# Kernel tuning notes

Measured on AMD Instinct MI355X. Metric: run time of the kernel, lower is better.

The kernel has to match this reference:

```python
import jax, jax.numpy as jnp
import numpy as np

TAU = 2.0          # LIF membrane time constant (spikingjelly default)
ALPHA = 2.0        # ATan surrogate width
EPS = 1e-5         # BatchNorm eps
NUM_HEADS = 8
SCALE = 0.125

@jax.custom_vjp
def spike(x):
    return (x >= 0.0).astype(x.dtype)

def _spike_fwd(x):
    return (x >= 0.0).astype(x.dtype), x

def _spike_bwd(x, g):
    # ATan surrogate gradient (spikingjelly default)
    return (g * (ALPHA / 2.0) / (1.0 + (jnp.pi / 2.0 * ALPHA * x) ** 2),)

spike.defvjp(_spike_fwd, _spike_bwd)

def lif(x, v_th):
    # Multi-step LIF over leading time axis T; hard reset to 0, v_reset=0.
    def step(v, xt):
        h = v + (xt - v) / TAU
        s = spike(h - v_th)
        return h * (1.0 - s), s
    _, s = jax.lax.scan(step, jnp.zeros_like(x[0]), x)
    return s

def bn(x, g, b, m, v):
    # BatchNorm1d in eval mode over channel (last) dim
    return (x - m) * jax.lax.rsqrt(v + EPS) * g + b

def setup_inputs() -> dict:
    key = jax.random.key(0)
    ks = jax.random.split(key, 16)
    T, B, N, C = 4, 16, 512, 512
    s = 1.0 / np.sqrt(C)
    inp = {"x": jax.random.normal(ks[0], (T, B, N, C), jnp.float32)}
    for i, p in enumerate("qkvp"):
        inp[f"w{p}"] = jax.random.normal(ks[1 + i], (C, C), jnp.float32) * s
        inp[f"b{p}"] = jnp.zeros((C,), jnp.float32)
        inp[f"{p}_gamma"] = jnp.ones((C,), jnp.float32)
        inp[f"{p}_beta"] = jnp.zeros((C,), jnp.float32)
        inp[f"{p}_mean"] = jax.random.normal(ks[5 + i], (C,), jnp.float32) * 0.1
        inp[f"{p}_var"] = jax.random.uniform(ks[9 + i], (C,), jnp.float32, minval=0.5, maxval=1.5)
    return inp

def reference(x, wq, bq, q_gamma, q_beta, q_mean, q_var,
              wk, bk, k_gamma, k_beta, k_mean, k_var,
              wv, bv, v_gamma, v_beta, v_mean, v_var,
              wp, bp, p_gamma, p_beta, p_mean, p_var):
    T, B, N, C = x.shape
    H = NUM_HEADS
    D = C // H

    def branch(w, b, g, be, m, va):
        y = bn(x @ w.T + b, g, be, m, va)          # Linear -> BN1d (eval)
        y = lif(y, 1.0)                             # spiking activation
        return y.reshape(T, B, N, H, D).transpose(0, 1, 3, 2, 4)  # [T,B,H,N,D]

    q = branch(wq, bq, q_gamma, q_beta, q_mean, q_var)
    k = branch(wk, bk, k_gamma, k_beta, k_mean, k_var)
    v = branch(wv, bv, v_gamma, v_beta, v_mean, v_var)

    attn = jnp.einsum('tbhnd,tbhmd->tbhnm', q, k) * SCALE  # [T,B,H,N,N]
    o = jnp.einsum('tbhnm,tbhmd->tbhnd', attn, v)          # [T,B,H,N,D]
    o = o.transpose(0, 1, 3, 2, 4).reshape(T, B, N, C)
    o = lif(o, 0.5)                                        # attn_lif, v_th=0.5
    o = bn(o @ wp.T + bp, p_gamma, p_beta, p_mean, p_var)
    return lif(o, 1.0)
```

## Files before the change

kernel.cpp:

```cpp
#include <hip/hip_runtime.h>
#include <hip/hip_bf16.h>
#include <hip/hip_fp16.h>
#include <cstddef>
#include <cstdint>

#define T_ 4
#define B_ 16
#define N_ 512
#define C_ 512
#define H_ 8
#define D_ 64
#define BN_T (B_*N_)

typedef unsigned short u16;
typedef __attribute__((ext_vector_type(8))) short bf16x8;
typedef __attribute__((ext_vector_type(8))) _Float16 f16x8;
typedef __attribute__((ext_vector_type(8))) unsigned short u16x8;
typedef __attribute__((ext_vector_type(4))) float f32x4;

__device__ __forceinline__ u16 f2bf_exact(float f) {
    union { float f; unsigned u; } x; x.f = f; return (u16)(x.u >> 16);
}
__device__ __forceinline__ void split2(float f, u16& h1, u16& h2) {
    const __half a = __float2half(f);
    const float r = (f - __half2float(a)) * 2048.0f;
    const __half b = __float2half(r);
    h1 = __half_as_ushort(a); h2 = __half_as_ushort(b);
}
__device__ __forceinline__ int swz(int rr, int q) {
    return (rr << 6) + (((q ^ ((rr >> 1) & 3)) & 3) << 4);
}
__device__ __forceinline__ int SW(int row, int col) {
    return (row << 6) + (col ^ ((row & 7) << 3));
}
__device__ __forceinline__ void gload16(const void* g, void* l) {
    __builtin_amdgcn_global_load_lds(
        (const __attribute__((address_space(1))) unsigned int*)g,
        (__attribute__((address_space(3))) unsigned int*)l, 16, 0, 0);
}

__global__ __launch_bounds__(256) void k_split_x(
    const float* __restrict__ x, u16* __restrict__ x1t, u16* __restrict__ x2t)
{
    const int tile = blockIdx.x;
    const int mt = tile >> 4, kb = tile & 15;
    const int tid = threadIdx.x;
    const int rr = tid >> 1, kh = tid & 1;
    const int t = rr & 3, bn = mt * 32 + (rr >> 2);
    const float* src = x + ((size_t)t * BN_T + bn) * C_ + kb * 32 + kh * 16;
    float f[16];
    *reinterpret_cast<float4*>(f + 0)  = *reinterpret_cast<const float4*>(src + 0);
    *reinterpret_cast<float4*>(f + 4)  = *reinterpret_cast<const float4*>(src + 4);
    *reinterpret_cast<float4*>(f + 8)  = *reinterpret_cast<const float4*>(src + 8);
    *reinterpret_cast<float4*>(f + 12) = *reinterpret_cast<const float4*>(src + 12);
    char* d1 = (char*)(x1t + ((size_t)tile << 12));
    char* d2 = (char*)(x2t + ((size_t)tile << 12));
    #pragma unroll
    for (int j = 0; j < 2; ++j) {
        u16x8 p1, p2;
        #pragma unroll
        for (int e = 0; e < 8; ++e) { u16 h1, h2; split2(f[8*j+e], h1, h2); p1[e] = h1; p2[e] = h2; }
        const int q = 2 * kh + j;
        *reinterpret_cast<u16x8*>(d1 + swz(rr, q)) = p1;
        *reinterpret_cast<u16x8*>(d2 + swz(rr, q)) = p2;
    }
}

__global__ __launch_bounds__(256) void k_split_w(
    const float* __restrict__ w, u16* __restrict__ w1t, u16* __restrict__ w2t)
{
    const int tile = blockIdx.x;
    const int nt = tile >> 4, kb = tile & 15;
    const int tid = threadIdx.x;
    const int rr = tid >> 1, kh = tid & 1;
    const int c = nt * 128 + rr;
    const float* src = w + (size_t)c * C_ + kb * 32 + kh * 16;
    float f[16];
    *reinterpret_cast<float4*>(f + 0)  = *reinterpret_cast<const float4*>(src + 0);
    *reinterpret_cast<float4*>(f + 4)  = *reinterpret_cast<const float4*>(src + 4);
    *reinterpret_cast<float4*>(f + 8)  = *reinterpret_cast<const float4*>(src + 8);
    *reinterpret_cast<float4*>(f + 12) = *reinterpret_cast<const float4*>(src + 12);
    char* d1 = (char*)(w1t + ((size_t)tile << 12));
    char* d2 = (char*)(w2t + ((size_t)tile << 12));
    #pragma unroll
    for (int j = 0; j < 2; ++j) {
        u16x8 p1, p2;
        #pragma unroll
        for (int e = 0; e < 8; ++e) { u16 h1, h2; split2(f[8*j+e], h1, h2); p1[e] = h1; p2[e] = h2; }
        const int q = 2 * kh + j;
        *reinterpret_cast<u16x8*>(d1 + swz(rr, q)) = p1;
        *reinterpret_cast<u16x8*>(d2 + swz(rr, q)) = p2;
    }
}

__global__ __launch_bounds__(256, 2) void k_linear_qkv(
    const u16* __restrict__ a1t, const u16* __restrict__ a2t,
    const u16* __restrict__ wt_base,
    const float* __restrict__ bi0, const float* __restrict__ ga0, const float* __restrict__ be0,
    const float* __restrict__ mu0, const float* __restrict__ va0,
    const float* __restrict__ bi1, const float* __restrict__ ga1, const float* __restrict__ be1,
    const float* __restrict__ mu1, const float* __restrict__ va1,
    const float* __restrict__ bi2, const float* __restrict__ ga2, const float* __restrict__ be2,
    const float* __restrict__ mu2, const float* __restrict__ va2,
    u16* __restrict__ oq, u16* __restrict__ ok, u16* __restrict__ ov)
{
    __shared__ u16 lds[2][2][4096];

    const int dd  = blockIdx.x;
    const int lid = (dd & 7) * 384 + (dd >> 3);
    const int mt  = lid / 12;
    const int ntg = lid - mt * 12;
    const int li  = ntg >> 2;
    const int nt  = ntg & 3;
    const int bn0 = mt * 32;
    const int c0  = nt * 128;

    const float* bias  = li == 0 ? bi0 : li == 1 ? bi1 : bi2;
    const float* gamma = li == 0 ? ga0 : li == 1 ? ga1 : ga2;
    const float* beta  = li == 0 ? be0 : li == 1 ? be1 : be2;
    const float* mean  = li == 0 ? mu0 : li == 1 ? mu1 : mu2;
    const float* var   = li == 0 ? va0 : li == 1 ? va1 : va2;
    u16* outp = li == 0 ? oq : li == 1 ? ok : ov;

    const size_t WSZ = (size_t)C_ * C_;
    const u16* w1t = wt_base + (size_t)(2 * li) * WSZ;
    const u16* w2t = wt_base + (size_t)(2 * li + 1) * WSZ;

    const int tid = threadIdx.x;
    const int wv  = tid >> 6, lane = tid & 63;
    const int l15 = tid & 15, g = (tid & 63) >> 4;
    const int wr  = wv >> 1, wc = wv & 1;
    const int go  = wv * 2048 + lane * 16;
    const int lo  = wv * 2048;

    f32x4 accA[4][4], accB[4][4];
    #pragma unroll
    for (int rt = 0; rt < 4; ++rt)
        #pragma unroll
        for (int ct = 0; ct < 4; ++ct) { accA[rt][ct] = {0,0,0,0}; accB[rt][ct] = {0,0,0,0}; }

    const size_t abase = (size_t)mt * 16, bbase = (size_t)nt * 16;

    auto stage = [&](int buf, int kb) {
        char* L = (char*)&lds[buf][0][0];
        const char* gb1 = (const char*)(w1t + ((bbase + kb) << 12)) + go;
        const char* gb2 = (const char*)(w2t + ((bbase + kb) << 12)) + go;
        gload16(gb1,        L + lo);
        gload16(gb1 + 1024, L + lo + 1024);
        gload16(gb2,        L + 8192 + lo);
        gload16(gb2 + 1024, L + 8192 + lo + 1024);
    };
    auto lda = [&](int kb, f16x8 (&a1)[4], f16x8 (&a2)[4]) {
        const char* t1 = (const char*)(a1t + ((abase + kb) << 12));
        const char* t2 = (const char*)(a2t + ((abase + kb) << 12));
        #pragma unroll
        for (int rt = 0; rt < 4; ++rt) {
            const int rr = 64 * wr + 16 * rt + l15;
            a1[rt] = *reinterpret_cast<const f16x8*>(t1 + swz(rr, g));
            a2[rt] = *reinterpret_cast<const f16x8*>(t2 + swz(rr, g));
        }
    };
    auto comp = [&](int buf, const f16x8 (&a1)[4], const f16x8 (&a2)[4]) {
        const char* L = (const char*)&lds[buf][0][0];
        #pragma unroll
        for (int ct = 0; ct < 4; ++ct) {
            const int rr2 = 64 * wc + 16 * ct + l15;
            const f16x8 b1 = *reinterpret_cast<const f16x8*>(L + swz(rr2, g));
            const f16x8 b2 = *reinterpret_cast<const f16x8*>(L + 8192 + swz(rr2, g));
            #pragma unroll
            for (int rt = 0; rt < 4; ++rt) {
                accA[rt][ct] = __builtin_amdgcn_mfma_f32_16x16x32_f16(a1[rt], b1, accA[rt][ct], 0, 0, 0);
                accB[rt][ct] = __builtin_amdgcn_mfma_f32_16x16x32_f16(a2[rt], b1, accB[rt][ct], 0, 0, 0);
                accB[rt][ct] = __builtin_amdgcn_mfma_f32_16x16x32_f16(a1[rt], b2, accB[rt][ct], 0, 0, 0);
            }
        }
    };

    f16x8 aE1[4], aE2[4], aO1[4], aO2[4];
    lda(0, aE1, aE2);
    stage(0, 0);
    __syncthreads();

    #pragma unroll 1
    for (int kb = 0; kb < 16; kb += 2) {
        lda(kb + 1, aO1, aO2);
        stage(1, kb + 1);
        comp(0, aE1, aE2);
        __syncthreads();
        if (kb + 2 < 16) { lda(kb + 2, aE1, aE2); stage(0, kb + 2); }
        comp(1, aO1, aO2);
        __syncthreads();
    }

    #pragma unroll
    for (int ct = 0; ct < 4; ++ct) {
        const int c = c0 + 64 * wc + 16 * ct + l15;
        const float rs = 1.0f / sqrtf(var[c] + 1e-5f);
        const float ga = gamma[c], be = beta[c], mu = mean[c], bi = bias[c];
        #pragma unroll
        for (int rt = 0; rt < 4; ++rt) {
            const int bn = bn0 + 16 * wr + 4 * rt + g;
            float vm = 0.f;
            #pragma unroll
            for (int r = 0; r < 4; ++r) {
                const float y = accA[rt][ct][r] + accB[rt][ct][r] * (1.0f / 2048.0f) + bi;
                const float ybn = (y - mu) * rs * ga + be;
                const float h = vm + (ybn - vm) * 0.5f;
                const bool sp = (h >= 1.0f);
                vm = sp ? 0.f : h;
                const int b = bn >> 9, n = bn & 511;
                const int hh = c >> 6, d2 = c & 63;
                outp[((((size_t)r * B_ + b) * H_ + hh) * N_ + n) * D_ + d2] = sp ? 0x3F80 : 0;
            }
        }
    }
}

__global__ __launch_bounds__(256, 2) void k_linear_out(
    const u16* __restrict__ a1t,
    const u16* __restrict__ w1t, const u16* __restrict__ w2t,
    const float* __restrict__ bias, const float* __restrict__ gamma,
    const float* __restrict__ beta, const float* __restrict__ mean,
    const float* __restrict__ var, float* __restrict__ outp)
{
    __shared__ u16 lds[2][2][4096];

    const int dd  = blockIdx.x;
    const int lid = (dd & 7) * 128 + (dd >> 3);
    const int mt  = lid >> 2;
    const int nt  = lid & 3;
    const int bn0 = mt * 32;
    const int c0  = nt * 128;

    const int tid = threadIdx.x;
    const int wv  = tid >> 6, lane = tid & 63;
    const int l15 = tid & 15, g = (tid & 63) >> 4;
    const int wr  = wv >> 1, wc = wv & 1;
    const int go  = wv * 2048 + lane * 16;
    const int lo  = wv * 2048;

    f32x4 accA[4][4], accB[4][4];
    #pragma unroll
    for (int rt = 0; rt < 4; ++rt)
        #pragma unroll
        for (int ct = 0; ct < 4; ++ct) { accA[rt][ct] = {0,0,0,0}; accB[rt][ct] = {0,0,0,0}; }

    const size_t abase = (size_t)mt * 16, bbase = (size_t)nt * 16;

    auto stage = [&](int buf, int kb) {
        char* L = (char*)&lds[buf][0][0];
        const char* gb1 = (const char*)(w1t + ((bbase + kb) << 12)) + go;
        const char* gb2 = (const char*)(w2t + ((bbase + kb) << 12)) + go;
        gload16(gb1,        L + lo);
        gload16(gb1 + 1024, L + lo + 1024);
        gload16(gb2,        L + 8192 + lo);
        gload16(gb2 + 1024, L + 8192 + lo + 1024);
    };
    auto lda = [&](int kb, f16x8 (&a1)[4]) {
        const char* t1 = (const char*)(a1t + ((abase + kb) << 12));
        #pragma unroll
        for (int rt = 0; rt < 4; ++rt) {
            const int rr = 64 * wr + 16 * rt + l15;
            a1[rt] = *reinterpret_cast<const f16x8*>(t1 + swz(rr, g));
        }
    };
    auto comp = [&](int buf, const f16x8 (&a1)[4]) {
        const char* L = (const char*)&lds[buf][0][0];
        #pragma unroll
        for (int ct = 0; ct < 4; ++ct) {
            const int rr2 = 64 * wc + 16 * ct + l15;
            const f16x8 b1 = *reinterpret_cast<const f16x8*>(L + swz(rr2, g));
            const f16x8 b2 = *reinterpret_cast<const f16x8*>(L + 8192 + swz(rr2, g));
            #pragma unroll
            for (int rt = 0; rt < 4; ++rt) {
                accA[rt][ct] = __builtin_amdgcn_mfma_f32_16x16x32_f16(a1[rt], b1, accA[rt][ct], 0, 0, 0);
                accB[rt][ct] = __builtin_amdgcn_mfma_f32_16x16x32_f16(a1[rt], b2, accB[rt][ct], 0, 0, 0);
            }
        }
    };

    f16x8 aE1[4], aO1[4];
    lda(0, aE1);
    stage(0, 0);
    __syncthreads();

    #pragma unroll 1
    for (int kb = 0; kb < 16; kb += 2) {
        lda(kb + 1, aO1);
        stage(1, kb + 1);
        comp(0, aE1);
        __syncthreads();
        if (kb + 2 < 16) { lda(kb + 2, aE1); stage(0, kb + 2); }
        comp(1, aO1);
        __syncthreads();
    }

    #pragma unroll
    for (int ct = 0; ct < 4; ++ct) {
        const int c = c0 + 64 * wc + 16 * ct + l15;
        const float rs = 1.0f / sqrtf(var[c] + 1e-5f);
        const float ga = gamma[c], be = beta[c], mu = mean[c], bi = bias[c];
        #pragma unroll
        for (int rt = 0; rt < 4; ++rt) {
            const int bn = bn0 + 16 * wr + 4 * rt + g;
            float vm = 0.f;
            #pragma unroll
            for (int r = 0; r < 4; ++r) {
                const float y = accA[rt][ct][r] + accB[rt][ct][r] * (1.0f / 2048.0f) + bi;
                const float ybn = (y - mu) * rs * ga + be;
                const float h = vm + (ybn - vm) * 0.5f;
                const bool sp = (h >= 1.0f);
                vm = sp ? 0.f : h;
                outp[((size_t)r * BN_T + bn) * C_ + c] = sp ? 1.0f : 0.0f;
            }
        }
    }
}

__global__ __launch_bounds__(512, 2) void k_attn_mfma(
    const u16* __restrict__ qg, const u16* __restrict__ kg,
    const u16* __restrict__ vg, u16* __restrict__ s2t)
{
    __shared__ u16 kf[8][4096];
    __shared__ u16 vf[8][4096];
    __shared__ u16 ssb[8][1024];

    const int id  = blockIdx.x;
    const int lid = (id & 7) * 64 + (id >> 3);
    const int bh  = lid >> 2;
    const int qt  = lid & 3;
    const int b   = bh >> 3, hh = bh & 7;

    const int tid  = threadIdx.x;
    const int w    = tid >> 6, lane = tid & 63;
    const int l15  = lane & 15, g = lane >> 4;

    const int vkv = (tid & 15) * 4;
    const int vd  = ((tid >> 4) & 15) * 4;

    bf16x8 qa[2];
    f32x4 vmem[4], oacc[4];
    #pragma unroll
    for (int d0 = 0; d0 < 4; ++d0) { vmem[d0] = {0,0,0,0}; oacc[d0] = {0,0,0,0}; }

    #pragma unroll 1
    for (int t = 0; t < T_; ++t) {
        const size_t base = ((size_t)t * (B_ * H_) + bh) * (size_t)(N_ * D_);
        if (t > 0) __syncthreads();

        {
            const size_t qrow = base + (size_t)(qt * 128 + 16 * w + l15) * D_;
            qa[0] = *reinterpret_cast<const bf16x8*>(qg + qrow + 8 * g);
            qa[1] = *reinterpret_cast<const bf16x8*>(qg + qrow + 32 + 8 * g);
        }
        {
            const u16* kb = kg + base;
            #pragma unroll
            for (int i = 0; i < 8; ++i) {
                const int r64 = tid >> 3;
                const int col = (tid & 7) * 8;
                const u16x8 v = *reinterpret_cast<const u16x8*>(kb + ((size_t)(tid + 512 * i)) * 8);
                *reinterpret_cast<u16x8*>(&kf[i][SW(r64, col)]) = v;
            }
        }
        {
            const u16* vb = vg + base;
            #pragma unroll
            for (int i = 0; i < 4; ++i) {
                const int jt = 2 * i + (tid >> 8);
                const int m0 = jt * 64;
                ushort4 r0 = *reinterpret_cast<const ushort4*>(vb + (size_t)(m0 + vkv + 0) * D_ + vd);
                ushort4 r1 = *reinterpret_cast<const ushort4*>(vb + (size_t)(m0 + vkv + 1) * D_ + vd);
                ushort4 r2 = *reinterpret_cast<const ushort4*>(vb + (size_t)(m0 + vkv + 2) * D_ + vd);
                ushort4 r3 = *reinterpret_cast<const ushort4*>(vb + (size_t)(m0 + vkv + 3) * D_ + vd);
                ushort4 wv4;
                wv4.x = r0.x; wv4.y = r1.x; wv4.z = r2.x; wv4.w = r3.x;
                *reinterpret_cast<ushort4*>(&vf[jt][SW(vd + 0, vkv)]) = wv4;
                wv4.x = r0.y; wv4.y = r1.y; wv4.z = r2.y; wv4.w = r3.y;
                *reinterpret_cast<ushort4*>(&vf[jt][SW(vd + 1, vkv)]) = wv4;
                wv4.x = r0.z; wv4.y = r1.z; wv4.z = r2.z; wv4.w = r3.z;
                *reinterpret_cast<ushort4*>(&vf[jt][SW(vd + 2, vkv)]) = wv4;
                wv4.x = r0.w; wv4.y = r1.w; wv4.z = r2.w; wv4.w = r3.w;
                *reinterpret_cast<ushort4*>(&vf[jt][SW(vd + 3, vkv)]) = wv4;
            }
        }
        __syncthreads();

        u16* sb = &ssb[w][0];
        #pragma unroll
        for (int jt = 0; jt < 8; ++jt) {
            __builtin_amdgcn_s_setprio(1);
            #pragma unroll
            for (int kvt = 0; kvt < 2; ++kvt) {
                f32x4 acc = {0.f, 0.f, 0.f, 0.f};
                #pragma unroll
                for (int c = 0; c < 2; ++c) {
                    const bf16x8 kb = *reinterpret_cast<const bf16x8*>(
                        &kf[jt][SW(16 * kvt + l15, 32 * c + 8 * g)]);
                    acc = __builtin_amdgcn_mfma_f32_16x16x32_bf16(qa[c], kb, acc, 0, 0, 0);
                }
                #pragma unroll
                for (int r = 0; r < 4; ++r)
                    sb[SW(4 * g + r, 16 * kvt + l15)] = f2bf_exact(acc[r]);
            }
            {
                const bf16x8 sa = *reinterpret_cast<const bf16x8*>(&sb[SW(l15, 8 * g)]);
                #pragma unroll
                for (int d0 = 0; d0 < 4; ++d0) {
                    const bf16x8 vb2 = *reinterpret_cast<const bf16x8*>(
                        &vf[jt][SW(16 * d0 + l15, 8 * g)]);
                    oacc[d0] = __builtin_amdgcn_mfma_f32_16x16x32_bf16(sa, vb2, oacc[d0], 0, 0, 0);
                }
            }
            #pragma unroll
            for (int kvt = 2; kvt < 4; ++kvt) {
                f32x4 acc = {0.f, 0.f, 0.f, 0.f};
                #pragma unroll
                for (int c = 0; c < 2; ++c) {
                    const bf16x8 kb = *reinterpret_cast<const bf16x8*>(
                        &kf[jt][SW(16 * kvt + l15, 32 * c + 8 * g)]);
                    acc = __builtin_amdgcn_mfma_f32_16x16x32_bf16(qa[c], kb, acc, 0, 0, 0);
                }
                #pragma unroll
                for (int r = 0; r < 4; ++r)
                    sb[SW(4 * g + r, 16 * kvt + l15)] = f2bf_exact(acc[r]);
            }
            {
                const bf16x8 sa = *reinterpret_cast<const bf16x8*>(&sb[SW(l15, 32 + 8 * g)]);
                #pragma unroll
                for (int d0 = 0; d0 < 4; ++d0) {
                    const bf16x8 vb2 = *reinterpret_cast<const bf16x8*>(
                        &vf[jt][SW(16 * d0 + l15, 32 + 8 * g)]);
                    oacc[d0] = __builtin_amdgcn_mfma_f32_16x16x32_bf16(sa, vb2, oacc[d0], 0, 0, 0);
                }
            }
            __builtin_amdgcn_s_setprio(0);
        }

        #pragma unroll
        for (int d0 = 0; d0 < 4; ++d0) {
            const int c = hh * 64 + d0 * 16 + l15;
            const int kb2 = c >> 5, kq = (c >> 3) & 3, e = c & 7;
            #pragma unroll
            for (int r = 0; r < 4; ++r) {
                const float o = oacc[d0][r] * 0.125f;
                const float h = vmem[d0][r] + (o - vmem[d0][r]) * 0.5f;
                const bool sp = (h >= 0.5f);
                vmem[d0][r] = sp ? 0.f : h;
                const int n = qt * 128 + 16 * w + 4 * g + r;
                const int bn = b * 512 + n;
                const int mt2 = bn >> 5;
                const int rr2 = (bn & 31) * 4 + t;
                const size_t off = (((size_t)mt2 * 16 + kb2) << 13) + (rr2 << 6)
                                 + (((kq ^ ((rr2 >> 1) & 3)) & 3) << 4) + (e << 1);
                *(u16*)((char*)s2t + off) = sp ? 0x3C00 : 0;
            }
            oacc[d0] = {0.f, 0.f, 0.f, 0.f};
        }
    }
}

extern "C" void kernel_launch(void* const* d_in, const int* in_sizes, int n_in,
                              void* d_out, int out_size, void* d_ws, size_t ws_size,
                              hipStream_t stream)
{
    const float* x = (const float*)d_in[0];
    const float* W[4]  = {(const float*)d_in[1],  (const float*)d_in[7],  (const float*)d_in[13], (const float*)d_in[19]};
    const float* Bi[4] = {(const float*)d_in[2],  (const float*)d_in[8],  (const float*)d_in[14], (const float*)d_in[20]};
    const float* Ga[4] = {(const float*)d_in[3],  (const float*)d_in[9],  (const float*)d_in[15], (const float*)d_in[21]};
    const float* Be[4] = {(const float*)d_in[4],  (const float*)d_in[10], (const float*)d_in[16], (const float*)d_in[22]};
    const float* Mu[4] = {(const float*)d_in[5],  (const float*)d_in[11], (const float*)d_in[17], (const float*)d_in[23]};
    const float* Va[4] = {(const float*)d_in[6],  (const float*)d_in[12], (const float*)d_in[18], (const float*)d_in[24]};

    const size_t SPK = (size_t)T_ * B_ * N_ * C_;
    const size_t WSZ = (size_t)C_ * C_;
    u16* qb  = (u16*)d_ws;
    u16* kbf = qb + SPK;
    u16* vbf = kbf + SPK;
    u16* x1t = vbf + SPK;
    u16* x2t = x1t + SPK;
    u16* wt  = x2t + SPK;
    u16* s2t = x1t;

    dim3 blk(256);
    k_split_x<<<4096, blk, 0, stream>>>(x, x1t, x2t);
    for (int i = 0; i < 4; ++i)
        k_split_w<<<64, blk, 0, stream>>>(W[i], wt + (2*i) * WSZ, wt + (2*i+1) * WSZ);

    k_linear_qkv<<<3072, blk, 0, stream>>>(x1t, x2t, wt,
        Bi[0], Ga[0], Be[0], Mu[0], Va[0],
        Bi[1], Ga[1], Be[1], Mu[1], Va[1],
        Bi[2], Ga[2], Be[2], Mu[2], Va[2],
        qb, kbf, vbf);
    k_attn_mfma<<<512, dim3(512), 0, stream>>>(qb, kbf, vbf, s2t);
    k_linear_out<<<1024, blk, 0, stream>>>(s2t, wt + 6*WSZ, wt + 7*WSZ,
        Bi[3], Ga[3], Be[3], Mu[3], Va[3], (float*)d_out);
}
```

Baseline: 305.4 us.

## Widen linear GEMM tiles to 512 threads with triple-buffered LDS pipeline

Both linear kernels now use 512-thread blocks covering 256 output columns, so each block reuses its A tile across twice as many columns. The A operand is staged through LDS alongside the split weights instead of being read directly from global memory into registers. The double-buffered loop becomes a three-stage ring using explicit vmcnt waits, raw s_barrier and setprio around the MFMA loops, so global loads overlap compute more deeply. The cost is much more LDS per block (up to 144 KB for qkv), which may limit occupancy, plus the risk of fragile hand-written waitcnt counts.

```diff
diff --git a/kernel.cpp b/kernel.cpp
--- a/kernel.cpp
+++ b/kernel.cpp
@@ -93,7 +93,7 @@
     }
 }
 
-__global__ __launch_bounds__(256, 2) void k_linear_qkv(
+__global__ __launch_bounds__(512, 2) void k_linear_qkv(
     const u16* __restrict__ a1t, const u16* __restrict__ a2t,
     const u16* __restrict__ wt_base,
     const float* __restrict__ bi0, const float* __restrict__ ga0, const float* __restrict__ be0,
@@ -104,16 +104,16 @@
     const float* __restrict__ mu2, const float* __restrict__ va2,
     u16* __restrict__ oq, u16* __restrict__ ok, u16* __restrict__ ov)
 {
-    __shared__ u16 lds[2][2][4096];
+    __shared__ u16 lds[3][6][4096];
 
     const int dd  = blockIdx.x;
-    const int lid = (dd & 7) * 384 + (dd >> 3);
-    const int mt  = lid / 12;
-    const int ntg = lid - mt * 12;
-    const int li  = ntg >> 2;
-    const int nt  = ntg & 3;
+    const int lid = (dd & 7) * 192 + (dd >> 3);
+    const int mt  = lid / 6;
+    const int rem = lid - mt * 6;
+    const int li  = rem >> 1;
+    const int nt  = rem & 1;
     const int bn0 = mt * 32;
-    const int c0  = nt * 128;
+    const int c0  = nt * 256;
 
     const float* bias  = li == 0 ? bi0 : li == 1 ? bi1 : bi2;
     const float* gamma = li == 0 ? ga0 : li == 1 ? ga1 : ga2;
@@ -128,10 +128,9 @@
 
     const int tid = threadIdx.x;
     const int wv  = tid >> 6, lane = tid & 63;
-    const int l15 = tid & 15, g = (tid & 63) >> 4;
-    const int wr  = wv >> 1, wc = wv & 1;
-    const int go  = wv * 2048 + lane * 16;
-    const int lo  = wv * 2048;
+    const int l15 = lane & 15, g = (lane >> 4) & 3;
+    const int wr  = wv >> 2, wc = wv & 3;
+    const int so  = tid * 16;
 
     f32x4 accA[4][4], accB[4][4];
     #pragma unroll
@@ -139,34 +138,36 @@
         #pragma unroll
         for (int ct = 0; ct < 4; ++ct) { accA[rt][ct] = {0,0,0,0}; accB[rt][ct] = {0,0,0,0}; }
 
-    const size_t abase = (size_t)mt * 16, bbase = (size_t)nt * 16;
+    const size_t abase  = (size_t)mt * 16;
+    const size_t bbase0 = (size_t)(nt * 2 + 0) * 16;
+    const size_t bbase1 = (size_t)(nt * 2 + 1) * 16;
 
     auto stage = [&](int buf, int kb) {
         char* L = (char*)&lds[buf][0][0];
-        const char* gb1 = (const char*)(w1t + ((bbase + kb) << 12)) + go;
-        const char* gb2 = (const char*)(w2t + ((bbase + kb) << 12)) + go;
-        gload16(gb1,        L + lo);
-        gload16(gb1 + 1024, L + lo + 1024);
-        gload16(gb2,        L + 8192 + lo);
-        gload16(gb2 + 1024, L + 8192 + lo + 1024);
+        gload16((const char*)(a1t + ((abase  + kb) << 12)) + so, L + 0 * 8192 + so);
+        gload16((const char*)(a2t + ((abase  + kb) << 12)) + so, L + 1 * 8192 + so);
+        gload16((const char*)(w1t + ((bbase0 + kb) << 12)) + so, L + 2 * 8192 + so);
+        gload16((const char*)(w1t + ((bbase1 + kb) << 12)) + so, L + 3 * 8192 + so);
+        gload16((const char*)(w2t + ((bbase0 + kb) << 12)) + so, L + 4 * 8192 + so);
+        gload16((const char*)(w2t + ((bbase1 + kb) << 12)) + so, L + 5 * 8192 + so);
     };
-    auto lda = [&](int kb, f16x8 (&a1)[4], f16x8 (&a2)[4]) {
-        const char* t1 = (const char*)(a1t + ((abase + kb) << 12));
-        const char* t2 = (const char*)(a2t + ((abase + kb) << 12));
+    auto comp = [&](int buf) {
+        const char* L = (const char*)&lds[buf][0][0];
+        f16x8 a1[4], a2[4];
         #pragma unroll
         for (int rt = 0; rt < 4; ++rt) {
             const int rr = 64 * wr + 16 * rt + l15;
-            a1[rt] = *reinterpret_cast<const f16x8*>(t1 + swz(rr, g));
-            a2[rt] = *reinterpret_cast<const f16x8*>(t2 + swz(rr, g));
-        }
-    };
-    auto comp = [&](int buf, const f16x8 (&a1)[4], const f16x8 (&a2)[4]) {
-        const char* L = (const char*)&lds[buf][0][0];
+            a1[rt] = *reinterpret_cast<const f16x8*>(L + 0 * 8192 + swz(rr, g));
+            a2[rt] = *reinterpret_cast<const f16x8*>(L + 1 * 8192 + swz(rr, g));
+        }
+        __builtin_amdgcn_s_setprio(1);
         #pragma unroll
         for (int ct = 0; ct < 4; ++ct) {
-            const int rr2 = 64 * wc + 16 * ct + l15;
-            const f16x8 b1 = *reinterpret_cast<const f16x8*>(L + swz(rr2, g));
-            const f16x8 b2 = *reinterpret_cast<const f16x8*>(L + 8192 + swz(rr2, g));
+            const int cc = 64 * wc + 16 * ct;
+            const int ub = 2 + (cc >> 7);
+            const int rrB = (cc & 127) + l15;
+            const f16x8 b1 = *reinterpret_cast<const f16x8*>(L + ub * 8192 + swz(rrB, g));
+            const f16x8 b2 = *reinterpret_cast<const f16x8*>(L + (ub + 2) * 8192 + swz(rrB, g));
             #pragma unroll
             for (int rt = 0; rt < 4; ++rt) {
                 accA[rt][ct] = __builtin_amdgcn_mfma_f32_16x16x32_f16(a1[rt], b1, accA[rt][ct], 0, 0, 0);
@@ -174,23 +175,31 @@
                 accB[rt][ct] = __builtin_amdgcn_mfma_f32_16x16x32_f16(a1[rt], b2, accB[rt][ct], 0, 0, 0);
             }
         }
+        __builtin_amdgcn_s_setprio(0);
     };
 
-    f16x8 aE1[4], aE2[4], aO1[4], aO2[4];
-    lda(0, aE1, aE2);
     stage(0, 0);
-    __syncthreads();
+    stage(1, 1);
+    __builtin_amdgcn_sched_barrier(0);
+    asm volatile("s_waitcnt vmcnt(6) lgkmcnt(0)" ::: "memory");
+    __builtin_amdgcn_s_barrier();
+    __builtin_amdgcn_sched_barrier(0);
 
     #pragma unroll 1
-    for (int kb = 0; kb < 16; kb += 2) {
-        lda(kb + 1, aO1, aO2);
-        stage(1, kb + 1);
-        comp(0, aE1, aE2);
-        __syncthreads();
-        if (kb + 2 < 16) { lda(kb + 2, aE1, aE2); stage(0, kb + 2); }
-        comp(1, aO1, aO2);
-        __syncthreads();
-    }
+    for (int k = 0; k < 14; ++k) {
+        stage((k + 2) % 3, k + 2);
+        comp(k % 3);
+        __builtin_amdgcn_sched_barrier(0);
+        asm volatile("s_waitcnt vmcnt(6) lgkmcnt(0)" ::: "memory");
+        __builtin_amdgcn_s_barrier();
+        __builtin_amdgcn_sched_barrier(0);
+    }
+    comp(14 % 3);
+    __builtin_amdgcn_sched_barrier(0);
+    asm volatile("s_waitcnt vmcnt(0) lgkmcnt(0)" ::: "memory");
+    __builtin_amdgcn_s_barrier();
+    __builtin_amdgcn_sched_barrier(0);
+    comp(15 % 3);
 
     #pragma unroll
     for (int ct = 0; ct < 4; ++ct) {
@@ -216,28 +225,27 @@
     }
 }
 
-__global__ __launch_bounds__(256, 2) void k_linear_out(
+__global__ __launch_bounds__(512, 2) void k_linear_out(
     const u16* __restrict__ a1t,
     const u16* __restrict__ w1t, const u16* __restrict__ w2t,
     const float* __restrict__ bias, const float* __restrict__ gamma,
     const float* __restrict__ beta, const float* __restrict__ mean,
     const float* __restrict__ var, float* __restrict__ outp)
 {
-    __shared__ u16 lds[2][2][4096];
+    __shared__ u16 lds[3][5][4096];
 
     const int dd  = blockIdx.x;
-    const int lid = (dd & 7) * 128 + (dd >> 3);
-    const int mt  = lid >> 2;
-    const int nt  = lid & 3;
+    const int lid = (dd & 7) * 64 + (dd >> 3);
+    const int mt  = lid >> 1;
+    const int nt  = lid & 1;
     const int bn0 = mt * 32;
-    const int c0  = nt * 128;
+    const int c0  = nt * 256;
 
     const int tid = threadIdx.x;
     const int wv  = tid >> 6, lane = tid & 63;
-    const int l15 = tid & 15, g = (tid & 63) >> 4;
-    const int wr  = wv >> 1, wc = wv & 1;
-    const int go  = wv * 2048 + lane * 16;
-    const int lo  = wv * 2048;
+    const int l15 = lane & 15, g = (lane >> 4) & 3;
+    const int wr  = wv >> 2, wc = wv & 3;
+    const int so  = tid * 16;
 
     f32x4 accA[4][4], accB[4][4];
     #pragma unroll
@@ -245,55 +253,65 @@
         #pragma unroll
         for (int ct = 0; ct < 4; ++ct) { accA[rt][ct] = {0,0,0,0}; accB[rt][ct] = {0,0,0,0}; }
 
-    const size_t abase = (size_t)mt * 16, bbase = (size_t)nt * 16;
+    const size_t abase  = (size_t)mt * 16;
+    const size_t bbase0 = (size_t)(nt * 2 + 0) * 16;
+    const size_t bbase1 = (size_t)(nt * 2 + 1) * 16;
 
     auto stage = [&](int buf, int kb) {
         char* L = (char*)&lds[buf][0][0];
-        const char* gb1 = (const char*)(w1t + ((bbase + kb) << 12)) + go;
-        const char* gb2 = (const char*)(w2t + ((bbase + kb) << 12)) + go;
-        gload16(gb1,        L + lo);
-        gload16(gb1 + 1024, L + lo + 1024);
-        gload16(gb2,        L + 8192 + lo);
-        gload16(gb2 + 1024, L + 8192 + lo + 1024);
+        gload16((const char*)(a1t + ((abase  + kb) << 12)) + so, L + 0 * 8192 + so);
+        gload16((const char*)(w1t + ((bbase0 + kb) << 12)) + so, L + 1 * 8192 + so);
+        gload16((const char*)(w1t + ((bbase1 + kb) << 12)) + so, L + 2 * 8192 + so);
+        gload16((const char*)(w2t + ((bbase0 + kb) << 12)) + so, L + 3 * 8192 + so);
+        gload16((const char*)(w2t + ((bbase1 + kb) << 12)) + so, L + 4 * 8192 + so);
     };
-    auto lda = [&](int kb, f16x8 (&a1)[4]) {
-        const char* t1 = (const char*)(a1t + ((abase + kb) << 12));
+    auto comp = [&](int buf) {
+        const char* L = (const char*)&lds[buf][0][0];
+        f16x8 a1[4];
         #pragma unroll
         for (int rt = 0; rt < 4; ++rt) {
             const int rr = 64 * wr + 16 * rt + l15;
-            a1[rt] = *reinterpret_cast<const f16x8*>(t1 + swz(rr, g));
-        }
-    };
-    auto comp = [&](int buf, const f16x8 (&a1)[4]) {
-        const char* L = (const char*)&lds[buf][0][0];
+            a1[rt] = *reinterpret_cast<const f16x8*>(L + 0 * 8192 + swz(rr, g));
+        }
+        __builtin_amdgcn_s_setprio(1);
         #pragma unroll
         for (int ct = 0; ct < 4; ++ct) {
-            const int rr2 = 64 * wc + 16 * ct + l15;
-            const f16x8 b1 = *reinterpret_cast<const f16x8*>(L + swz(rr2, g));
-            const f16x8 b2 = *reinterpret_cast<const f16x8*>(L + 8192 + swz(rr2, g));
+            const int cc = 64 * wc + 16 * ct;
+            const int ub = 1 + (cc >> 7);
+            const int rrB = (cc & 127) + l15;
+            const f16x8 b1 = *reinterpret_cast<const f16x8*>(L + ub * 8192 + swz(rrB, g));
+            const f16x8 b2 = *reinterpret_cast<const f16x8*>(L + (ub + 2) * 8192 + swz(rrB, g));
             #pragma unroll
             for (int rt = 0; rt < 4; ++rt) {
                 accA[rt][ct] = __builtin_amdgcn_mfma_f32_16x16x32_f16(a1[rt], b1, accA[rt][ct], 0, 0, 0);
                 accB[rt][ct] = __builtin_amdgcn_mfma_f32_16x16x32_f16(a1[rt], b2, accB[rt][ct], 0, 0, 0);
             }
         }
+        __builtin_amdgcn_s_setprio(0);
     };
 
-    f16x8 aE1[4], aO1[4];
-    lda(0, aE1);
     stage(0, 0);
-    __syncthreads();
+    stage(1, 1);
+    __builtin_amdgcn_sched_barrier(0);
+    asm volatile("s_waitcnt vmcnt(5) lgkmcnt(0)" ::: "memory");
+    __builtin_amdgcn_s_barrier();
+    __builtin_amdgcn_sched_barrier(0);
 
     #pragma unroll 1
-    for (int kb = 0; kb < 16; kb += 2) {
-        lda(kb + 1, aO1);
-        stage(1, kb + 1);
-        comp(0, aE1);
-        __syncthreads();
-        if (kb + 2 < 16) { lda(kb + 2, aE1); stage(0, kb + 2); }
-        comp(1, aO1);
-        __syncthreads();
-    }
+    for (int k = 0; k < 14; ++k) {
+        stage((k + 2) % 3, k + 2);
+        comp(k % 3);
+        __builtin_amdgcn_sched_barrier(0);
+        asm volatile("s_waitcnt vmcnt(5) lgkmcnt(0)" ::: "memory");
+        __builtin_amdgcn_s_barrier();
+        __builtin_amdgcn_sched_barrier(0);
+    }
+    comp(14 % 3);
+    __builtin_amdgcn_sched_barrier(0);
+    asm volatile("s_waitcnt vmcnt(0) lgkmcnt(0)" ::: "memory");
+    __builtin_amdgcn_s_barrier();
+    __builtin_amdgcn_sched_barrier(0);
+    comp(15 % 3);
 
     #pragma unroll
     for (int ct = 0; ct < 4; ++ct) {
@@ -487,12 +505,12 @@
     for (int i = 0; i < 4; ++i)
         k_split_w<<<64, blk, 0, stream>>>(W[i], wt + (2*i) * WSZ, wt + (2*i+1) * WSZ);
 
-    k_linear_qkv<<<3072, blk, 0, stream>>>(x1t, x2t, wt,
+    k_linear_qkv<<<1536, dim3(512), 0, stream>>>(x1t, x2t, wt,
         Bi[0], Ga[0], Be[0], Mu[0], Va[0],
         Bi[1], Ga[1], Be[1], Mu[1], Va[1],
         Bi[2], Ga[2], Be[2], Mu[2], Va[2],
         qb, kbf, vbf);
     k_attn_mfma<<<512, dim3(512), 0, stream>>>(qb, kbf, vbf, s2t);
-    k_linear_out<<<1024, blk, 0, stream>>>(s2t, wt + 6*WSZ, wt + 7*WSZ,
+    k_linear_out<<<512, dim3(512), 0, stream>>>(s2t, wt + 6*WSZ, wt + 7*WSZ,
         Bi[3], Ga[3], Be[3], Mu[3], Va[3], (float*)d_out);
 }
```

Result: no change. 300.7 us (-1.5%).
